# Performance work log

Hardware: AMD Instinct MI355X
Metric: run time of the kernel (lower is better)

The kernel has to match this reference:

```python
import jax, jax.numpy as jnp
import numpy as np
import math

B = 128      # n_atom_basis
F = 32       # n_filters
R = 20       # n_rbf
N = 16384    # atoms
E = 262144   # edges
LOG2 = 0.6931471805599453
IS2 = 1.0 / math.sqrt(2.0)
IS3 = 1.0 / math.sqrt(3.0)
IS6 = 1.0 / math.sqrt(6.0)


def ssp(x):
    # shifted softplus: softplus(x) - log(2)
    return jax.nn.softplus(x) - LOG2


def setup_inputs() -> dict:
    key = jax.random.key(0)
    ks = jax.random.split(key, 14)
    return dict(
        x=jax.random.normal(ks[0], (N, 4 * B), jnp.float32),
        idx_i=jax.random.randint(ks[1], (E,), 0, N),
        idx_j=jax.random.randint(ks[2], (E,), 0, N),
        f_ij=jax.random.normal(ks[3], (E, R), jnp.float32),
        rcut_ij=jax.random.uniform(ks[4], (E,), jnp.float32),
        Yr_ij=jax.random.normal(ks[5], (E, 4), jnp.float32),
        # e3nn-style Linear weights (N(0,1), normalized by 1/sqrt(fan_in) at use)
        w_in2f_s=jax.random.normal(ks[6], (B, F), jnp.float32),
        w_in2f_v=jax.random.normal(ks[7], (B, F), jnp.float32),
        W1=jax.random.normal(ks[8], (R, F), jnp.float32) / math.sqrt(R),
        b1=jnp.zeros((F,), jnp.float32),
        W2=jax.random.normal(ks[9], (F, 6 * F), jnp.float32) / math.sqrt(F),
        b2=jnp.zeros((6 * F,), jnp.float32),
        w_f2o1_s=jax.random.normal(ks[10], (2 * F, B), jnp.float32),
        w_f2o1_v=jax.random.normal(ks[11], (2 * F, B), jnp.float32),
        w_f2o2_s=jax.random.normal(ks[12], (B, B), jnp.float32),
        w_f2o2_v=jax.random.normal(ks[13], (B, B), jnp.float32),
    )


def reference(x, idx_i, idx_j, f_ij, rcut_ij, Yr_ij,
              w_in2f_s, w_in2f_v, W1, b1, W2, b2,
              w_f2o1_s, w_f2o1_v, w_f2o2_s, w_f2o2_v):
    n = x.shape[0]
    # input layout: [B x 0e | B x 1o]
    xs = x[:, :B]                          # [N,B] scalars
    xv = x[:, B:].reshape(n, B, 3)         # [N,B,3] vectors
    # in2f: per-l equivariant linear (fan_in = B)
    hs = (xs @ w_in2f_s) / math.sqrt(B)                            # [N,F]
    hv = jnp.einsum('nbc,bf->nfc', xv, w_in2f_v) / math.sqrt(B)    # [N,F,3]
    # gather neighbors j
    s = hs[idx_j]                          # [E,F]
    v = hv[idx_j]                          # [E,F,3]
    ys = Yr_ij[:, 0]                       # [E]   l=0 part of Y(r)
    yv = Yr_ij[:, 1:4]                     # [E,3] l=1 part of Y(r)
    # FullTensorProduct (0e+1o) x (0e+1o), component normalization
    t_s1 = s * ys[:, None]                                   # 0e (0x0)
    t_s2 = jnp.einsum('efc,ec->ef', v, yv) * IS3             # 0e (1x1->0)
    t_v1 = s[:, :, None] * yv[:, None, :]                    # 1o (0x1)
    t_v2 = v * ys[:, None, None]                             # 1o (1x0)
    t_pv = jnp.cross(v, yv[:, None, :]) * IS2                # 1e (1x1->1)
    ax, ay, az = v[..., 0], v[..., 1], v[..., 2]
    bx, by, bz = yv[:, None, 0:1], yv[:, None, 1:2], yv[:, None, 2:3]
    bx, by, bz = bx[..., 0], by[..., 0], bz[..., 0]
    t_q = jnp.stack([                                        # 2e (1x1->2)
        (ax * by + ay * bx) * IS2,
        (ay * bz + az * by) * IS2,
        (2.0 * az * bz - ax * bx - ay * by) * IS6,
        (ax * bz + az * bx) * IS2,
        (ax * bx - ay * by) * IS2,
    ], axis=-1)                                              # [E,F,5]
    # radial filter network -> one scalar per irrep instance (6 per filter)
    h = ssp(f_ij @ W1 + b1)
    Wij = (h @ W2 + b2) * rcut_ij[:, None]                   # [E,6F]
    Wf = Wij.reshape(-1, F, 6)
    # elementwise tensor product (continuous-filter convolution)
    edge = jnp.concatenate([
        (t_s1 * Wf[..., 0])[..., None],
        (t_s2 * Wf[..., 1])[..., None],
        t_v1 * Wf[..., 2:3],
        t_v2 * Wf[..., 3:4],
        t_pv * Wf[..., 4:5],
        t_q * Wf[..., 5:6],
    ], axis=-1)                                              # [E,F,16]
    # scatter-add over center atoms i
    agg = jax.ops.segment_sum(edge.reshape(edge.shape[0], -1), idx_i,
                              num_segments=n).reshape(n, F, 16)
    # f2out_1: e3nn Linear keeps only matching irreps (0e,1o); 1e,2e dropped
    s_in = jnp.concatenate([agg[..., 0], agg[..., 1]], axis=1)          # [N,2F]
    v_in = jnp.concatenate([agg[..., 2:5], agg[..., 5:8]], axis=1)      # [N,2F,3]
    os1 = (s_in @ w_f2o1_s) / math.sqrt(2 * F)
    ov1 = jnp.einsum('nmc,mb->nbc', v_in, w_f2o1_v) / math.sqrt(2 * F)
    # gated activation: ssp on scalars only
    os1 = ssp(os1)
    # f2out_2
    os2 = (os1 @ w_f2o2_s) / math.sqrt(B)
    ov2 = jnp.einsum('nbc,bd->ndc', ov1, w_f2o2_v) / math.sqrt(B)
    return jnp.concatenate([os2, ov2.reshape(n, -1)], axis=-1)          # [N,4B]
```

## Files before the change

kernel.cpp:

```cpp
#include <hip/hip_runtime.h>
#include <math.h>

#define NN 16384
#define BB 128
#define FF 32
#define RR 20
#define EE 262144

typedef __attribute__((ext_vector_type(8))) short bf16x8;
typedef __attribute__((ext_vector_type(4))) float f32x4;

__device__ __forceinline__ float sspf(float x) {
  float t = __expf(-fabsf(x));
  return fmaxf(x, 0.0f) + (__log2f(1.0f + t) - 1.0f) * 0.69314718055994531f;
}

__device__ __forceinline__ unsigned int pack_bf2(float a, float b) {
  unsigned int ua = __float_as_uint(a);
  ua = (ua + 0x7fffu + ((ua >> 16) & 1u)) >> 16;
  unsigned int ub = __float_as_uint(b);
  ub = (ub + 0x7fffu + ((ub >> 16) & 1u)) & 0xffff0000u;
  return ua | ub;
}

__device__ __forceinline__ unsigned short pack_bf1(float a) {
  unsigned int ua = __float_as_uint(a);
  ua = (ua + 0x7fffu + ((ua >> 16) & 1u)) >> 16;
  return (unsigned short)ua;
}

__global__ __launch_bounds__(256) void k_embed(const float* __restrict__ x,
        const float* __restrict__ ws, const float* __restrict__ wv,
        float4* __restrict__ hsv) {
  __shared__ float sx[32 * 516];
  int t = threadIdx.x;
  int b0 = blockIdx.x * 32;
  const float4* xg = (const float4*)(x + (size_t)b0 * 512);
  for (int i = t; i < 4096; i += 256) {
    int row = i >> 7, col = i & 127;
    *(float4*)(sx + row * 516 + col * 4) = xg[i];
  }
  __syncthreads();
  int n = t >> 3, fq = t & 7;
  const float* xr = sx + n * 516;
  float acc[4][4];
#pragma unroll
  for (int k = 0; k < 4; k++)
#pragma unroll
    for (int c = 0; c < 4; c++) acc[k][c] = 0.f;
  for (int bq = 0; bq < 32; bq++) {
    float4 xs4 = *(const float4*)(xr + 4 * bq);
    float4 a0 = *(const float4*)(xr + 128 + 12 * bq);
    float4 a1 = *(const float4*)(xr + 128 + 12 * bq + 4);
    float4 a2 = *(const float4*)(xr + 128 + 12 * bq + 8);
    float xsv[4] = {xs4.x, xs4.y, xs4.z, xs4.w};
    float vv[4][3];
    vv[0][0] = a0.x; vv[0][1] = a0.y; vv[0][2] = a0.z;
    vv[1][0] = a0.w; vv[1][1] = a1.x; vv[1][2] = a1.y;
    vv[2][0] = a1.z; vv[2][1] = a1.w; vv[2][2] = a2.x;
    vv[3][0] = a2.y; vv[3][1] = a2.z; vv[3][2] = a2.w;
#pragma unroll
    for (int bb = 0; bb < 4; bb++) {
      int b = 4 * bq + bb;
      float4 w_s = *(const float4*)(ws + b * 32 + 4 * fq);
      float4 w_v = *(const float4*)(wv + b * 32 + 4 * fq);
      float wsx[4] = {w_s.x, w_s.y, w_s.z, w_s.w};
      float wvx[4] = {w_v.x, w_v.y, w_v.z, w_v.w};
#pragma unroll
      for (int k = 0; k < 4; k++) {
        acc[k][0] += xsv[bb] * wsx[k];
        acc[k][1] += vv[bb][0] * wvx[k];
        acc[k][2] += vv[bb][1] * wvx[k];
        acc[k][3] += vv[bb][2] * wvx[k];
      }
    }
  }
  const float sc = 0.088388347648318447f;
#pragma unroll
  for (int k = 0; k < 4; k++) {
    float4 o;
    o.x = acc[k][0] * sc; o.y = acc[k][1] * sc;
    o.z = acc[k][2] * sc; o.w = acc[k][3] * sc;
    hsv[(size_t)(b0 + n) * 32 + 4 * fq + k] = o;
  }
}

__global__ __launch_bounds__(256) void k_count(const int* __restrict__ idx_i,
        int* __restrict__ cnt, int* __restrict__ pos) {
  int e = blockIdx.x * 256 + threadIdx.x;
  pos[e] = atomicAdd(cnt + idx_i[e], 1);
}

__global__ __launch_bounds__(256) void k_scan(const int* __restrict__ cnt,
        int* __restrict__ offs) {
  __shared__ int part[256];
  int t = threadIdx.x;
  int s = 0;
  for (int i = t * 64; i < t * 64 + 64; ++i) s += cnt[i];
  part[t] = s;
  __syncthreads();
  if (t == 0) {
    int run = 0;
    for (int i = 0; i < 256; i++) { int v = part[i]; part[i] = run; run += v; }
    offs[NN] = run;
  }
  __syncthreads();
  int run = part[t];
  for (int i = t * 64; i < t * 64 + 64; ++i) { offs[i] = run; run += cnt[i]; }
}

__global__ __launch_bounds__(256) void k_fill(const int* __restrict__ idx_i,
        const int* __restrict__ idx_j, const float* __restrict__ Yr,
        const int* __restrict__ pos, const int* __restrict__ offs,
        int* __restrict__ slot_of_e, int* __restrict__ idxj_csr,
        float4* __restrict__ Yr_csr) {
  int e = blockIdx.x * 256 + threadIdx.x;
  int slot = offs[idx_i[e]] + pos[e];
  slot_of_e[e] = slot;
  idxj_csr[slot] = idx_j[e];
  Yr_csr[slot] = *(const float4*)(Yr + (size_t)e * 4);
}

__global__ __launch_bounds__(256) void k_wv(const float* __restrict__ w1v,
        const float* __restrict__ w2v, float* __restrict__ Wv) {
  int o = blockIdx.x * 256 + threadIdx.x;
  int m = o >> 7, d = o & 127;
  float s = 0.f;
  for (int b = 0; b < 128; b++) s += w1v[m * 128 + b] * w2v[b * 128 + d];
  Wv[o] = s * 0.011048543456039804f;
}

__global__ __launch_bounds__(256) void k_prep(const float* __restrict__ W2,
        unsigned short* __restrict__ BTbf) {
  int i = blockIdx.x * 256 + threadIdx.x;
  int col = i >> 5, k = i & 31;
  BTbf[col * 32 + k] = pack_bf1(W2[k * 192 + 6 * (col >> 2) + (col & 3)]);
}

__global__ __launch_bounds__(256, 4) void k_wab(
        const float* __restrict__ fij, const float* __restrict__ rcut,
        const int* __restrict__ slot_of_e,
        const float* __restrict__ W1, const float* __restrict__ b1,
        const unsigned short* __restrict__ BTbf, const float* __restrict__ b2,
        unsigned int* __restrict__ Wab) {
  __shared__ float sfij[20 * 130];
  __shared__ unsigned short hbf[128 * 40];
  __shared__ float sW1[640];
  __shared__ float sb1[32];
  __shared__ float sb2c[128];
  __shared__ float srct[128];
  __shared__ int sslot[128];
  int t = threadIdx.x;
  size_t e0 = (size_t)blockIdx.x * 128;
  for (int i = t; i < 640; i += 256) sW1[i] = W1[i];
  if (t < 32) sb1[t] = b1[t];
  if (t < 128) {
    sb2c[t] = b2[6 * (t >> 2) + (t & 3)];
    srct[t] = rcut[e0 + t];
    sslot[t] = slot_of_e[e0 + t];
  }
  for (int i = t; i < 2560; i += 256) {
    int el = i / 20, r = i - el * 20;
    sfij[r * 130 + el] = fij[e0 * 20 + i];
  }
  __syncthreads();
  {
    int el = t >> 1, fp0 = (t & 1) * 16;
    float acc[16];
#pragma unroll
    for (int i = 0; i < 16; i++) acc[i] = sb1[fp0 + i];
#pragma unroll
    for (int r = 0; r < 20; r++) {
      float fe = sfij[r * 130 + el];
      float4 wA = *(const float4*)(sW1 + r * 32 + fp0);
      float4 wB = *(const float4*)(sW1 + r * 32 + fp0 + 4);
      float4 wC = *(const float4*)(sW1 + r * 32 + fp0 + 8);
      float4 wD = *(const float4*)(sW1 + r * 32 + fp0 + 12);
      acc[0] += fe * wA.x;  acc[1] += fe * wA.y;
      acc[2] += fe * wA.z;  acc[3] += fe * wA.w;
      acc[4] += fe * wB.x;  acc[5] += fe * wB.y;
      acc[6] += fe * wB.z;  acc[7] += fe * wB.w;
      acc[8] += fe * wC.x;  acc[9] += fe * wC.y;
      acc[10] += fe * wC.z; acc[11] += fe * wC.w;
      acc[12] += fe * wD.x; acc[13] += fe * wD.y;
      acc[14] += fe * wD.z; acc[15] += fe * wD.w;
    }
    unsigned int* hw = (unsigned int*)hbf;
#pragma unroll
    for (int i = 0; i < 8; i++)
      hw[el * 20 + (fp0 >> 1) + i] =
          pack_bf2(sspf(acc[2 * i]), sspf(acc[2 * i + 1]));
  }
  __syncthreads();
  {
    int w = t >> 6, l = t & 63;
    int lrow = l & 15, lq = l >> 4;
    int lkq = lq * 8;
    bf16x8 bfr[8];
#pragma unroll
    for (int g = 0; g < 8; g++)
      bfr[g] = *(const bf16x8*)(BTbf + (g * 16 + lrow) * 32 + lkq);
#pragma unroll
    for (int et2 = 0; et2 < 2; et2++) {
      int edge = (2 * w + et2) * 16 + lrow;
      bf16x8 af = *(const bf16x8*)(hbf + edge * 40 + lkq);
      float rc = srct[edge];
      unsigned int* dst = Wab + (size_t)sslot[edge] * 64;
#pragma unroll
      for (int g = 0; g < 8; g++) {
        f32x4 z = {0.f, 0.f, 0.f, 0.f};
        f32x4 acc = __builtin_amdgcn_mfma_f32_16x16x32_bf16(bfr[g], af, z, 0, 0, 0);
        float4 bias = *(const float4*)(sb2c + g * 16 + lq * 4);
        uint2 o;
        o.x = pack_bf2((acc[0] + bias.x) * rc, (acc[1] + bias.y) * rc);
        o.y = pack_bf2((acc[2] + bias.z) * rc, (acc[3] + bias.w) * rc);
        *(uint2*)(dst + g * 8 + lq * 2) = o;
      }
    }
  }
}

__global__ __launch_bounds__(256, 4) void k_agg3(
        const unsigned int* __restrict__ Wu, const int* __restrict__ idxj_csr,
        const float4* __restrict__ Yr_csr, const float4* __restrict__ hsv,
        const int* __restrict__ offs, float* __restrict__ nagg) {
  int t = threadIdx.x;
  int w = t >> 6, l = t & 63;
  int n = blockIdx.x * 4 + w;
  int f = l >> 1, kb = (l & 1) * 2;
  int start = offs[n], end = offs[n + 1];
  float a0 = 0, a1 = 0, a2 = 0, a3 = 0, a4 = 0, a5 = 0;
  if (start < end) {
    int last = end - 1;
    int i1 = start + 1 < last ? start + 1 : last;
    int i2 = start + 2 < last ? start + 2 : last;
    int j0 = idxj_csr[start];
    int j1 = idxj_csr[i1];
    int j2 = idxj_csr[i2];
    float4 y0 = Yr_csr[start];
    float4 sv0 = hsv[(size_t)j0 * 32 + f];
    float4 sv1 = hsv[(size_t)j1 * 32 + f];
    unsigned int W0 = Wu[(size_t)start * 64 + l];
    unsigned int W1 = Wu[(size_t)i1 * 64 + l];
    for (int ei = start; ei < end; ++ei) {
      int in1 = ei + 1 < last ? ei + 1 : last;
      int in2 = ei + 2 < last ? ei + 2 : last;
      int in3 = ei + 3 < last ? ei + 3 : last;
      float4 sv2 = hsv[(size_t)j2 * 32 + f];
      unsigned int W2r = Wu[(size_t)in2 * 64 + l];
      float4 y1 = Yr_csr[in1];
      int j3 = idxj_csr[in3];
      float Wx = __uint_as_float(W0 << 16);
      float Wy = __uint_as_float(W0 & 0xffff0000u);
      float ys = y0.x, yx = y0.y, yy = y0.z, yz = y0.w;
      float ss = sv0.x, vx = sv0.y, vy = sv0.z, vz = sv0.w;
      if (kb == 0) {
        a0 += ss * ys * Wx;
        a1 += (vx * yx + vy * yy + vz * yz) * 0.57735026918962576f * Wy;
      } else {
        a0 += ss * yx * Wx; a1 += ss * yy * Wx; a2 += ss * yz * Wx;
        a3 += vx * ys * Wy; a4 += vy * ys * Wy; a5 += vz * ys * Wy;
      }
      y0 = y1; sv0 = sv1; sv1 = sv2; W0 = W1; W1 = W2r; j2 = j3;
    }
  }
  float* na = nagg + (size_t)n * 256;
  if (kb == 0) {
    na[f] = a0;
    na[32 + f] = a1;
  } else {
    na[64 + 3 * f + 0] = a0;  na[64 + 3 * f + 1] = a1;  na[64 + 3 * f + 2] = a2;
    na[160 + 3 * f + 0] = a3; na[160 + 3 * f + 1] = a4; na[160 + 3 * f + 2] = a5;
  }
}

__global__ __launch_bounds__(256) void k_os1(const float* __restrict__ na,
        const float* __restrict__ w1s, float* __restrict__ os1) {
  __shared__ float sw[8192];
  int t = threadIdx.x;
  for (int i = t; i < 8192; i += 256) sw[i] = w1s[i];
  __syncthreads();
  int dg = t & 31, ng = t >> 5;
  int d0 = dg * 4;
  int n0 = blockIdx.x * 32 + ng * 4;
  const float* ap = na + (size_t)n0 * 256;
  float acc[4][4] = {};
#pragma unroll
  for (int kq = 0; kq < 16; kq++) {
    float4 a[4];
#pragma unroll
    for (int j = 0; j < 4; j++) a[j] = *(const float4*)(ap + j * 256 + 4 * kq);
    float4 w0 = *(const float4*)(sw + (4 * kq + 0) * 128 + d0);
    float4 w1 = *(const float4*)(sw + (4 * kq + 1) * 128 + d0);
    float4 w2 = *(const float4*)(sw + (4 * kq + 2) * 128 + d0);
    float4 w3 = *(const float4*)(sw + (4 * kq + 3) * 128 + d0);
#pragma unroll
    for (int j = 0; j < 4; j++) {
      acc[j][0] += a[j].x * w0.x + a[j].y * w1.x + a[j].z * w2.x + a[j].w * w3.x;
      acc[j][1] += a[j].x * w0.y + a[j].y * w1.y + a[j].z * w2.y + a[j].w * w3.y;
      acc[j][2] += a[j].x * w0.z + a[j].y * w1.z + a[j].z * w2.z + a[j].w * w3.z;
      acc[j][3] += a[j].x * w0.w + a[j].y * w1.w + a[j].z * w2.w + a[j].w * w3.w;
    }
  }
#pragma unroll
  for (int j = 0; j < 4; j++) {
    float4 o;
    o.x = sspf(acc[j][0] * 0.125f);
    o.y = sspf(acc[j][1] * 0.125f);
    o.z = sspf(acc[j][2] * 0.125f);
    o.w = sspf(acc[j][3] * 0.125f);
    *(float4*)(os1 + (size_t)(n0 + j) * 128 + d0) = o;
  }
}

__global__ __launch_bounds__(256) void k_os2(const float* __restrict__ os1,
        const float* __restrict__ w2s, float* __restrict__ out) {
  __shared__ float sw[16384];
  int t = threadIdx.x;
  for (int i = t; i < 16384; i += 256) sw[i] = w2s[i];
  __syncthreads();
  int dg = t & 31, ng = t >> 5;
  int d0 = dg * 4;
  int n0 = blockIdx.x * 32 + ng * 4;
  const float* ap = os1 + (size_t)n0 * 128;
  float acc[4][4] = {};
#pragma unroll
  for (int kq = 0; kq < 32; kq++) {
    float4 a[4];
#pragma unroll
    for (int j = 0; j < 4; j++) a[j] = *(const float4*)(ap + j * 128 + 4 * kq);
    float4 w0 = *(const float4*)(sw + (4 * kq + 0) * 128 + d0);
    float4 w1 = *(const float4*)(sw + (4 * kq + 1) * 128 + d0);
    float4 w2 = *(const float4*)(sw + (4 * kq + 2) * 128 + d0);
    float4 w3 = *(const float4*)(sw + (4 * kq + 3) * 128 + d0);
#pragma unroll
    for (int j = 0; j < 4; j++) {
      acc[j][0] += a[j].x * w0.x + a[j].y * w1.x + a[j].z * w2.x + a[j].w * w3.x;
      acc[j][1] += a[j].x * w0.y + a[j].y * w1.y + a[j].z * w2.y + a[j].w * w3.y;
      acc[j][2] += a[j].x * w0.z + a[j].y * w1.z + a[j].z * w2.z + a[j].w * w3.z;
      acc[j][3] += a[j].x * w0.w + a[j].y * w1.w + a[j].z * w2.w + a[j].w * w3.w;
    }
  }
  const float sc = 0.088388347648318447f;
#pragma unroll
  for (int j = 0; j < 4; j++) {
    float4 o;
    o.x = acc[j][0] * sc; o.y = acc[j][1] * sc;
    o.z = acc[j][2] * sc; o.w = acc[j][3] * sc;
    *(float4*)(out + (size_t)(n0 + j) * 512 + d0) = o;
  }
}

__global__ __launch_bounds__(256) void k_ov(const float* __restrict__ na,
        const float* __restrict__ Wv, float* __restrict__ out) {
  __shared__ float sw[8192];
  int t = threadIdx.x;
  for (int i = t; i < 8192; i += 256) sw[i] = Wv[i];
  __syncthreads();
  int dg = t & 31, ng = t >> 5;
  int d0 = dg * 4;
  int n0 = blockIdx.x * 16 + ng * 2;
  const float* ap = na + (size_t)n0 * 256 + 64;
  float acc[2][12] = {};
#pragma unroll
  for (int mq = 0; mq < 16; mq++) {
    float4 p[2][3];
#pragma unroll
    for (int j = 0; j < 2; j++) {
      p[j][0] = *(const float4*)(ap + j * 256 + 12 * mq);
      p[j][1] = *(const float4*)(ap + j * 256 + 12 * mq + 4);
      p[j][2] = *(const float4*)(ap + j * 256 + 12 * mq + 8);
    }
    float4 w0 = *(const float4*)(sw + (4 * mq + 0) * 128 + d0);
    float4 w1 = *(const float4*)(sw + (4 * mq + 1) * 128 + d0);
    float4 w2 = *(const float4*)(sw + (4 * mq + 2) * 128 + d0);
    float4 w3 = *(const float4*)(sw + (4 * mq + 3) * 128 + d0);
#pragma unroll
    for (int j = 0; j < 2; j++) {
      float vm[4][3];
      vm[0][0] = p[j][0].x; vm[0][1] = p[j][0].y; vm[0][2] = p[j][0].z;
      vm[1][0] = p[j][0].w; vm[1][1] = p[j][1].x; vm[1][2] = p[j][1].y;
      vm[2][0] = p[j][1].z; vm[2][1] = p[j][1].w; vm[2][2] = p[j][2].x;
      vm[3][0] = p[j][2].y; vm[3][1] = p[j][2].z; vm[3][2] = p[j][2].w;
      float wm[4][4];
      wm[0][0] = w0.x; wm[0][1] = w0.y; wm[0][2] = w0.z; wm[0][3] = w0.w;
      wm[1][0] = w1.x; wm[1][1] = w1.y; wm[1][2] = w1.z; wm[1][3] = w1.w;
      wm[2][0] = w2.x; wm[2][1] = w2.y; wm[2][2] = w2.z; wm[2][3] = w2.w;
      wm[3][0] = w3.x; wm[3][1] = w3.y; wm[3][2] = w3.z; wm[3][3] = w3.w;
#pragma unroll
      for (int m = 0; m < 4; m++)
#pragma unroll
        for (int i = 0; i < 4; i++)
#pragma unroll
          for (int c = 0; c < 3; c++)
            acc[j][i * 3 + c] += vm[m][c] * wm[m][i];
    }
  }
#pragma unroll
  for (int j = 0; j < 2; j++) {
    float* op = out + (size_t)(n0 + j) * 512 + 128 + 12 * dg;
    float4 o0, o1, o2;
    o0.x = acc[j][0]; o0.y = acc[j][1]; o0.z = acc[j][2]; o0.w = acc[j][3];
    o1.x = acc[j][4]; o1.y = acc[j][5]; o1.z = acc[j][6]; o1.w = acc[j][7];
    o2.x = acc[j][8]; o2.y = acc[j][9]; o2.z = acc[j][10]; o2.w = acc[j][11];
    *(float4*)op = o0;
    *(float4*)(op + 4) = o1;
    *(float4*)(op + 8) = o2;
  }
}

extern "C" void kernel_launch(void* const* d_in, const int* in_sizes, int n_in,
                              void* d_out, int out_size, void* d_ws, size_t ws_size,
                              hipStream_t stream) {
  const float* x    = (const float*)d_in[0];
  const int*   idx_i = (const int*)d_in[1];
  const int*   idx_j = (const int*)d_in[2];
  const float* fij  = (const float*)d_in[3];
  const float* rcut = (const float*)d_in[4];
  const float* Yr   = (const float*)d_in[5];
  const float* w_s  = (const float*)d_in[6];
  const float* w_v  = (const float*)d_in[7];
  const float* W1   = (const float*)d_in[8];
  const float* b1   = (const float*)d_in[9];
  const float* W2   = (const float*)d_in[10];
  const float* b2   = (const float*)d_in[11];
  const float* w1s  = (const float*)d_in[12];
  const float* w1v  = (const float*)d_in[13];
  const float* w2s  = (const float*)d_in[14];
  const float* w2v  = (const float*)d_in[15];
  float* out = (float*)d_out;

  char* ws = (char*)d_ws;
  size_t off = 0;
  auto alloc = [&](size_t bytes) {
    void* p = ws + off;
    off += (bytes + 255) & ~(size_t)255;
    return p;
  };
  float4* hsv   = (float4*)alloc((size_t)NN * 32 * 16);
  float*  nagg  = (float*)alloc((size_t)NN * 256 * 4);
  unsigned int* Wab = (unsigned int*)alloc((size_t)EE * 128 * 2);
  float*  os1   = (float*)alloc((size_t)NN * 128 * 4);
  float4* Yr_csr = (float4*)alloc((size_t)EE * 16);
  int* idxj_csr = (int*)alloc((size_t)EE * 4);
  int* slot_of_e = (int*)alloc((size_t)EE * 4);
  float* Wv     = (float*)alloc((size_t)8192 * 4);
  unsigned short* BTbf = (unsigned short*)alloc((size_t)4096 * 2);
  int* cnt      = (int*)alloc((size_t)NN * 4);
  int* offs     = (int*)alloc((size_t)(NN + 1) * 4);
  int* pos      = (int*)alloc((size_t)EE * 4);

  hipMemsetAsync(cnt, 0, (size_t)NN * 4, stream);
  k_count<<<EE / 256, 256, 0, stream>>>(idx_i, cnt, pos);
  k_scan<<<1, 256, 0, stream>>>(cnt, offs);
  k_fill<<<EE / 256, 256, 0, stream>>>(idx_i, idx_j, Yr, pos, offs,
                                       slot_of_e, idxj_csr, Yr_csr);
  k_embed<<<NN / 32, 256, 0, stream>>>(x, w_s, w_v, hsv);
  k_wv<<<32, 256, 0, stream>>>(w1v, w2v, Wv);
  k_prep<<<16, 256, 0, stream>>>(W2, BTbf);
  k_wab<<<EE / 128, 256, 0, stream>>>(fij, rcut, slot_of_e, W1, b1, BTbf, b2, Wab);
  k_agg3<<<NN / 4, 256, 0, stream>>>(Wab, idxj_csr, Yr_csr, hsv, offs, nagg);
  k_os1<<<512, 256, 0, stream>>>(nagg, w1s, os1);
  k_os2<<<512, 256, 0, stream>>>(os1, w2s, out);
  k_ov<<<1024, 256, 0, stream>>>(nagg, Wv, out);
}
```

Measured before the change: 194.4 us.

## Fuse filter-weight generation with CSR aggregation using per-run atomics

```diff
diff --git a/kernel.cpp b/kernel.cpp
--- a/kernel.cpp
+++ b/kernel.cpp
@@ -111,14 +111,19 @@
 
 __global__ __launch_bounds__(256) void k_fill(const int* __restrict__ idx_i,
         const int* __restrict__ idx_j, const float* __restrict__ Yr,
+        const float* __restrict__ rcut,
         const int* __restrict__ pos, const int* __restrict__ offs,
-        int* __restrict__ slot_of_e, int* __restrict__ idxj_csr,
-        float4* __restrict__ Yr_csr) {
+        int* __restrict__ elist, int* __restrict__ idxj_csr,
+        float4* __restrict__ Yr_csr, float* __restrict__ rcut_csr,
+        int* __restrict__ snode_g) {
   int e = blockIdx.x * 256 + threadIdx.x;
-  int slot = offs[idx_i[e]] + pos[e];
-  slot_of_e[e] = slot;
+  int ni = idx_i[e];
+  int slot = offs[ni] + pos[e];
+  elist[slot] = e;
   idxj_csr[slot] = idx_j[e];
   Yr_csr[slot] = *(const float4*)(Yr + (size_t)e * 4);
+  rcut_csr[slot] = rcut[e];
+  snode_g[slot] = ni;
 }
 
 __global__ __launch_bounds__(256) void k_wv(const float* __restrict__ w1v,
@@ -137,57 +142,60 @@
   BTbf[col * 32 + k] = pack_bf1(W2[k * 192 + 6 * (col >> 2) + (col & 3)]);
 }
 
-__global__ __launch_bounds__(256, 4) void k_wab(
-        const float* __restrict__ fij, const float* __restrict__ rcut,
-        const int* __restrict__ slot_of_e,
+__global__ __launch_bounds__(256, 4) void k_wagg(
+        const float* __restrict__ fij, const float* __restrict__ rcut_csr,
+        const int* __restrict__ elist,
         const float* __restrict__ W1, const float* __restrict__ b1,
         const unsigned short* __restrict__ BTbf, const float* __restrict__ b2,
-        unsigned int* __restrict__ Wab) {
-  __shared__ float sfij[20 * 130];
-  __shared__ unsigned short hbf[128 * 40];
+        const float4* __restrict__ Yr_csr, const int* __restrict__ idxj_csr,
+        const int* __restrict__ snode_g, const float4* __restrict__ hsv,
+        float* __restrict__ nagg) {
+  __shared__ char smem[16896];
+  __shared__ unsigned short hbf[64 * 40];
   __shared__ float sW1[640];
   __shared__ float sb1[32];
   __shared__ float sb2c[128];
-  __shared__ float srct[128];
-  __shared__ int sslot[128];
-  int t = threadIdx.x;
-  size_t e0 = (size_t)blockIdx.x * 128;
+  __shared__ float srct[64];
+  __shared__ float4 sYr[64];
+  __shared__ int sidxj[64];
+  __shared__ int snl[64];
+  float* sfij = (float*)smem;
+  unsigned short* swab = (unsigned short*)smem;
+  int t = threadIdx.x;
+  int s0 = blockIdx.x * 64;
   for (int i = t; i < 640; i += 256) sW1[i] = W1[i];
   if (t < 32) sb1[t] = b1[t];
-  if (t < 128) {
-    sb2c[t] = b2[6 * (t >> 2) + (t & 3)];
-    srct[t] = rcut[e0 + t];
-    sslot[t] = slot_of_e[e0 + t];
-  }
-  for (int i = t; i < 2560; i += 256) {
+  if (t < 128) sb2c[t] = b2[6 * (t >> 2) + (t & 3)];
+  if (t < 64) {
+    srct[t] = rcut_csr[s0 + t];
+    sidxj[t] = idxj_csr[s0 + t];
+    snl[t] = snode_g[s0 + t];
+    sYr[t] = Yr_csr[s0 + t];
+  }
+  for (int i = t; i < 1280; i += 256) {
     int el = i / 20, r = i - el * 20;
-    sfij[r * 130 + el] = fij[e0 * 20 + i];
+    int e = elist[s0 + el];
+    sfij[r * 66 + el] = fij[(size_t)e * 20 + r];
   }
   __syncthreads();
   {
-    int el = t >> 1, fp0 = (t & 1) * 16;
-    float acc[16];
-#pragma unroll
-    for (int i = 0; i < 16; i++) acc[i] = sb1[fp0 + i];
+    int el = t >> 2, fp0 = (t & 3) * 8;
+    float acc[8];
+#pragma unroll
+    for (int i = 0; i < 8; i++) acc[i] = sb1[fp0 + i];
 #pragma unroll
     for (int r = 0; r < 20; r++) {
-      float fe = sfij[r * 130 + el];
+      float fe = sfij[r * 66 + el];
       float4 wA = *(const float4*)(sW1 + r * 32 + fp0);
       float4 wB = *(const float4*)(sW1 + r * 32 + fp0 + 4);
-      float4 wC = *(const float4*)(sW1 + r * 32 + fp0 + 8);
-      float4 wD = *(const float4*)(sW1 + r * 32 + fp0 + 12);
-      acc[0] += fe * wA.x;  acc[1] += fe * wA.y;
-      acc[2] += fe * wA.z;  acc[3] += fe * wA.w;
-      acc[4] += fe * wB.x;  acc[5] += fe * wB.y;
-      acc[6] += fe * wB.z;  acc[7] += fe * wB.w;
-      acc[8] += fe * wC.x;  acc[9] += fe * wC.y;
-      acc[10] += fe * wC.z; acc[11] += fe * wC.w;
-      acc[12] += fe * wD.x; acc[13] += fe * wD.y;
-      acc[14] += fe * wD.z; acc[15] += fe * wD.w;
+      acc[0] += fe * wA.x; acc[1] += fe * wA.y;
+      acc[2] += fe * wA.z; acc[3] += fe * wA.w;
+      acc[4] += fe * wB.x; acc[5] += fe * wB.y;
+      acc[6] += fe * wB.z; acc[7] += fe * wB.w;
     }
     unsigned int* hw = (unsigned int*)hbf;
 #pragma unroll
-    for (int i = 0; i < 8; i++)
+    for (int i = 0; i < 4; i++)
       hw[el * 20 + (fp0 >> 1) + i] =
           pack_bf2(sspf(acc[2 * i]), sspf(acc[2 * i + 1]));
   }
@@ -200,59 +208,54 @@
 #pragma unroll
     for (int g = 0; g < 8; g++)
       bfr[g] = *(const bf16x8*)(BTbf + (g * 16 + lrow) * 32 + lkq);
-#pragma unroll
-    for (int et2 = 0; et2 < 2; et2++) {
-      int edge = (2 * w + et2) * 16 + lrow;
-      bf16x8 af = *(const bf16x8*)(hbf + edge * 40 + lkq);
-      float rc = srct[edge];
-      unsigned int* dst = Wab + (size_t)sslot[edge] * 64;
-#pragma unroll
-      for (int g = 0; g < 8; g++) {
-        f32x4 z = {0.f, 0.f, 0.f, 0.f};
-        f32x4 acc = __builtin_amdgcn_mfma_f32_16x16x32_bf16(bfr[g], af, z, 0, 0, 0);
-        float4 bias = *(const float4*)(sb2c + g * 16 + lq * 4);
-        uint2 o;
-        o.x = pack_bf2((acc[0] + bias.x) * rc, (acc[1] + bias.y) * rc);
-        o.y = pack_bf2((acc[2] + bias.z) * rc, (acc[3] + bias.w) * rc);
-        *(uint2*)(dst + g * 8 + lq * 2) = o;
+    int edge = w * 16 + lrow;
+    bf16x8 af = *(const bf16x8*)(hbf + edge * 40 + lkq);
+    float rc = srct[edge];
+#pragma unroll
+    for (int g = 0; g < 8; g++) {
+      f32x4 z = {0.f, 0.f, 0.f, 0.f};
+      f32x4 acc = __builtin_amdgcn_mfma_f32_16x16x32_bf16(bfr[g], af, z, 0, 0, 0);
+      float4 bias = *(const float4*)(sb2c + g * 16 + lq * 4);
+      uint2 o;
+      o.x = pack_bf2((acc[0] + bias.x) * rc, (acc[1] + bias.y) * rc);
+      o.y = pack_bf2((acc[2] + bias.z) * rc, (acc[3] + bias.w) * rc);
+      *(uint2*)(swab + edge * 132 + g * 16 + lq * 4) = o;
+    }
+  }
+  __syncthreads();
+  {
+    int w = t >> 6, l = t & 63;
+    int f = l >> 1, kb = (l & 1) * 2;
+    int base = w * 16;
+    float a0 = 0, a1 = 0, a2 = 0, a3 = 0, a4 = 0, a5 = 0;
+    int cur = snl[base];
+    float4 sv0 = hsv[(size_t)sidxj[base] * 32 + f];
+    float4 sv1 = hsv[(size_t)sidxj[base + 1] * 32 + f];
+    for (int i = 0; i < 16; ++i) {
+      int i2 = i + 2 < 16 ? i + 2 : 15;
+      float4 sv2 = hsv[(size_t)sidxj[base + i2] * 32 + f];
+      int slot = base + i;
+      int n = snl[slot];
+      if (n != cur) {
+        float* na = nagg + (size_t)cur * 256;
+        if (kb == 0) {
+          atomicAdd(na + f, a0); atomicAdd(na + 32 + f, a1);
+        } else {
+          atomicAdd(na + 64 + 3 * f + 0, a0);
+          atomicAdd(na + 64 + 3 * f + 1, a1);
+          atomicAdd(na + 64 + 3 * f + 2, a2);
+          atomicAdd(na + 160 + 3 * f + 0, a3);
+          atomicAdd(na + 160 + 3 * f + 1, a4);
+          atomicAdd(na + 160 + 3 * f + 2, a5);
+        }
+        a0 = a1 = a2 = a3 = a4 = a5 = 0.f;
+        cur = n;
       }
-    }
-  }
-}
-
-__global__ __launch_bounds__(256, 4) void k_agg3(
-        const unsigned int* __restrict__ Wu, const int* __restrict__ idxj_csr,
-        const float4* __restrict__ Yr_csr, const float4* __restrict__ hsv,
-        const int* __restrict__ offs, float* __restrict__ nagg) {
-  int t = threadIdx.x;
-  int w = t >> 6, l = t & 63;
-  int n = blockIdx.x * 4 + w;
-  int f = l >> 1, kb = (l & 1) * 2;
-  int start = offs[n], end = offs[n + 1];
-  float a0 = 0, a1 = 0, a2 = 0, a3 = 0, a4 = 0, a5 = 0;
-  if (start < end) {
-    int last = end - 1;
-    int i1 = start + 1 < last ? start + 1 : last;
-    int i2 = start + 2 < last ? start + 2 : last;
-    int j0 = idxj_csr[start];
-    int j1 = idxj_csr[i1];
-    int j2 = idxj_csr[i2];
-    float4 y0 = Yr_csr[start];
-    float4 sv0 = hsv[(size_t)j0 * 32 + f];
-    float4 sv1 = hsv[(size_t)j1 * 32 + f];
-    unsigned int W0 = Wu[(size_t)start * 64 + l];
-    unsigned int W1 = Wu[(size_t)i1 * 64 + l];
-    for (int ei = start; ei < end; ++ei) {
-      int in1 = ei + 1 < last ? ei + 1 : last;
-      int in2 = ei + 2 < last ? ei + 2 : last;
-      int in3 = ei + 3 < last ? ei + 3 : last;
-      float4 sv2 = hsv[(size_t)j2 * 32 + f];
-      unsigned int W2r = Wu[(size_t)in2 * 64 + l];
-      float4 y1 = Yr_csr[in1];
-      int j3 = idxj_csr[in3];
-      float Wx = __uint_as_float(W0 << 16);
-      float Wy = __uint_as_float(W0 & 0xffff0000u);
-      float ys = y0.x, yx = y0.y, yy = y0.z, yz = y0.w;
+      unsigned int W = *(const unsigned int*)(swab + slot * 132 + 2 * l);
+      float Wx = __uint_as_float(W << 16);
+      float Wy = __uint_as_float(W & 0xffff0000u);
+      float4 y = sYr[slot];
+      float ys = y.x, yx = y.y, yy = y.z, yz = y.w;
       float ss = sv0.x, vx = sv0.y, vy = sv0.z, vz = sv0.w;
       if (kb == 0) {
         a0 += ss * ys * Wx;
@@ -261,16 +264,19 @@
         a0 += ss * yx * Wx; a1 += ss * yy * Wx; a2 += ss * yz * Wx;
         a3 += vx * ys * Wy; a4 += vy * ys * Wy; a5 += vz * ys * Wy;
       }
-      y0 = y1; sv0 = sv1; sv1 = sv2; W0 = W1; W1 = W2r; j2 = j3;
-    }
-  }
-  float* na = nagg + (size_t)n * 256;
-  if (kb == 0) {
-    na[f] = a0;
-    na[32 + f] = a1;
-  } else {
-    na[64 + 3 * f + 0] = a0;  na[64 + 3 * f + 1] = a1;  na[64 + 3 * f + 2] = a2;
-    na[160 + 3 * f + 0] = a3; na[160 + 3 * f + 1] = a4; na[160 + 3 * f + 2] = a5;
+      sv0 = sv1; sv1 = sv2;
+    }
+    float* na = nagg + (size_t)cur * 256;
+    if (kb == 0) {
+      atomicAdd(na + f, a0); atomicAdd(na + 32 + f, a1);
+    } else {
+      atomicAdd(na + 64 + 3 * f + 0, a0);
+      atomicAdd(na + 64 + 3 * f + 1, a1);
+      atomicAdd(na + 64 + 3 * f + 2, a2);
+      atomicAdd(na + 160 + 3 * f + 0, a3);
+      atomicAdd(na + 160 + 3 * f + 1, a4);
+      atomicAdd(na + 160 + 3 * f + 2, a5);
+    }
   }
 }
 
@@ -439,11 +445,12 @@
   };
   float4* hsv   = (float4*)alloc((size_t)NN * 32 * 16);
   float*  nagg  = (float*)alloc((size_t)NN * 256 * 4);
-  unsigned int* Wab = (unsigned int*)alloc((size_t)EE * 128 * 2);
   float*  os1   = (float*)alloc((size_t)NN * 128 * 4);
   float4* Yr_csr = (float4*)alloc((size_t)EE * 16);
   int* idxj_csr = (int*)alloc((size_t)EE * 4);
-  int* slot_of_e = (int*)alloc((size_t)EE * 4);
+  int* elist    = (int*)alloc((size_t)EE * 4);
+  float* rcut_csr = (float*)alloc((size_t)EE * 4);
+  int* snode_g  = (int*)alloc((size_t)EE * 4);
   float* Wv     = (float*)alloc((size_t)8192 * 4);
   unsigned short* BTbf = (unsigned short*)alloc((size_t)4096 * 2);
   int* cnt      = (int*)alloc((size_t)NN * 4);
@@ -451,15 +458,17 @@
   int* pos      = (int*)alloc((size_t)EE * 4);
 
   hipMemsetAsync(cnt, 0, (size_t)NN * 4, stream);
+  hipMemsetAsync(nagg, 0, (size_t)NN * 256 * 4, stream);
   k_count<<<EE / 256, 256, 0, stream>>>(idx_i, cnt, pos);
   k_scan<<<1, 256, 0, stream>>>(cnt, offs);
-  k_fill<<<EE / 256, 256, 0, stream>>>(idx_i, idx_j, Yr, pos, offs,
-                                       slot_of_e, idxj_csr, Yr_csr);
+  k_fill<<<EE / 256, 256, 0, stream>>>(idx_i, idx_j, Yr, rcut, pos, offs,
+                                       elist, idxj_csr, Yr_csr, rcut_csr,
+                                       snode_g);
   k_embed<<<NN / 32, 256, 0, stream>>>(x, w_s, w_v, hsv);
   k_wv<<<32, 256, 0, stream>>>(w1v, w2v, Wv);
   k_prep<<<16, 256, 0, stream>>>(W2, BTbf);
-  k_wab<<<EE / 128, 256, 0, stream>>>(fij, rcut, slot_of_e, W1, b1, BTbf, b2, Wab);
-  k_agg3<<<NN / 4, 256, 0, stream>>>(Wab, idxj_csr, Yr_csr, hsv, offs, nagg);
+  k_wagg<<<EE / 64, 256, 0, stream>>>(fij, rcut_csr, elist, W1, b1, BTbf, b2,
+                                      Yr_csr, idxj_csr, snode_g, hsv, nagg);
   k_os1<<<512, 256, 0, stream>>>(nagg, w1s, os1);
   k_os2<<<512, 256, 0, stream>>>(os1, w2s, out);
   k_ov<<<1024, 256, 0, stream>>>(nagg, Wv, out);
```

Result: slower. 228.0 us (+17.3%).
